# Optimization experiments

Measured on AMD Instinct MI355X. Metric: run time of the kernel, lower is better.

The kernel has to match this reference:

```python
import jax, jax.numpy as jnp
import numpy as np

HIDDEN_SIZE = 2048
NUM_Q_HEADS = 16
NUM_KV_HEADS = 4
HEAD_DIM = 128
EPS = 1e-6
B, T = 1, 4096


def rms_norm(x, w):
    xf = x.astype(jnp.float32)
    n = xf * jax.lax.rsqrt(jnp.mean(xf * xf, axis=-1, keepdims=True) + EPS)
    return (n * w.astype(jnp.float32)).astype(x.dtype)


def rotate_half(x):
    x1, x2 = jnp.split(x, 2, axis=-1)
    return jnp.concatenate([-x2, x1], axis=-1)


def apply_rope(x, cos, sin):
    # x: [B, H, T, D]; cos/sin: [B, T, D]
    return x * cos[:, None, :, :] + rotate_half(x) * sin[:, None, :, :]


def setup_inputs() -> dict:
    key = jax.random.key(0)
    ks = jax.random.split(key, 6)
    s = 0.02
    x = jax.random.normal(ks[0], (B, T, HIDDEN_SIZE), dtype=jnp.float32)
    position_ids = jnp.arange(T, dtype=jnp.int64 if jax.config.jax_enable_x64 else jnp.int32)[None, :].repeat(B, axis=0)
    inv_freq = (1.0 / (10000.0 ** (np.arange(0, HEAD_DIM, 2, dtype=np.float32) / HEAD_DIM))).astype(np.float32)
    inv_freq = jnp.asarray(inv_freq)
    Wq = jax.random.normal(ks[1], (HIDDEN_SIZE, NUM_Q_HEADS * HEAD_DIM * 2), dtype=jnp.float32) * s
    Wk = jax.random.normal(ks[2], (HIDDEN_SIZE, NUM_KV_HEADS * HEAD_DIM), dtype=jnp.float32) * s
    Wv = jax.random.normal(ks[3], (HIDDEN_SIZE, NUM_KV_HEADS * HEAD_DIM), dtype=jnp.float32) * s
    Wo = jax.random.normal(ks[4], (NUM_Q_HEADS * HEAD_DIM, HIDDEN_SIZE), dtype=jnp.float32) * s
    q_norm_w = jnp.ones((HEAD_DIM,), dtype=jnp.float32)
    k_norm_w = jnp.ones((HEAD_DIM,), dtype=jnp.float32)
    return {"x": x, "position_ids": position_ids, "inv_freq": inv_freq,
            "Wq": Wq, "Wk": Wk, "Wv": Wv, "Wo": Wo,
            "q_norm_w": q_norm_w, "k_norm_w": k_norm_w}


def reference(x, position_ids, inv_freq, Wq, Wk, Wv, Wo, q_norm_w, k_norm_w):
    Bb, Tt, _ = x.shape
    dtype = x.dtype
    qg = (x @ Wq).reshape(Bb, Tt, NUM_Q_HEADS, HEAD_DIM * 2)
    q, gate = qg[..., :HEAD_DIM], qg[..., HEAD_DIM:]
    gate = gate.reshape(Bb, Tt, NUM_Q_HEADS * HEAD_DIM)
    k = (x @ Wk).reshape(Bb, Tt, NUM_KV_HEADS, HEAD_DIM)
    v = (x @ Wv).reshape(Bb, Tt, NUM_KV_HEADS, HEAD_DIM)
    q = rms_norm(q, q_norm_w)
    k = rms_norm(k, k_norm_w)
    q = q.transpose(0, 2, 1, 3)  # [B, Hq, T, D]
    k = k.transpose(0, 2, 1, 3)  # [B, Hkv, T, D]
    v = v.transpose(0, 2, 1, 3)
    # RoPE angles: [B, T, D/2] -> concat -> [B, T, D]
    freqs = position_ids.astype(jnp.float32)[:, :, None] * inv_freq[None, None, :]
    emb = jnp.concatenate([freqs, freqs], axis=-1)
    cos, sin = jnp.cos(emb).astype(dtype), jnp.sin(emb).astype(dtype)
    q = apply_rope(q, cos, sin)
    k = apply_rope(k, cos, sin)
    groups = NUM_Q_HEADS // NUM_KV_HEADS
    k = jnp.repeat(k, groups, axis=1)  # [B, Hq, T, D]
    v = jnp.repeat(v, groups, axis=1)
    scale = HEAD_DIM ** -0.5
    attn = jnp.einsum('bhqd,bhkd->bhqk', q, k) * scale
    causal = jnp.tril(jnp.ones((Tt, Tt), dtype=bool))
    attn = jnp.where(causal[None, None, :, :], attn, jnp.array(-jnp.inf, dtype=attn.dtype))
    attn = jax.nn.softmax(attn.astype(jnp.float32), axis=-1).astype(dtype)
    out = jnp.einsum('bhqk,bhkd->bhqd', attn, v)
    out = out.transpose(0, 2, 1, 3).reshape(Bb, Tt, NUM_Q_HEADS * HEAD_DIM)
    out = out * jax.nn.sigmoid(gate)
    return out @ Wo
```

## Files before the change

### kernel.cpp

```cpp
#include <hip/hip_runtime.h>
#include <hip/hip_bf16.h>

#define T_SEQ 4096
#define HID 2048
#define NQH 16
#define NKVH 4
#define HD 128
#define KVW (NKVH * HD)
#define KVSTRIDE 1024
#define QGW (NQH * HD * 2)

typedef __attribute__((ext_vector_type(8))) short short8;
typedef __attribute__((ext_vector_type(4))) float f32x4;
typedef __attribute__((ext_vector_type(16))) float f32x16;
typedef __hip_bfloat16 bf16;

__device__ inline float bf2f(bf16 v) { return __bfloat162float(v); }
__device__ inline bf16 f2bf(float v) { return __float2bfloat16(v); }

__device__ inline void storeC(float* p, float v) { *p = v; }
__device__ inline void storeC(bf16* p, float v) { *p = f2bf(v); }

#if __has_builtin(__builtin_amdgcn_exp2f)
__device__ inline float fexp2(float x) { return __builtin_amdgcn_exp2f(x); }
#else
extern "C" __device__ float __ocml_native_exp2_f32(float);
__device__ inline float fexp2(float x) { return __ocml_native_exp2_f32(x); }
#endif

__device__ inline void gload16(const void* g, void* l) {
    __builtin_amdgcn_global_load_lds(
        (const __attribute__((address_space(1))) void*)g,
        (__attribute__((address_space(3))) void*)l, 16, 0, 0);
}

__device__ inline unsigned pack2(float a, float b) {
    union { bf16 h[2]; unsigned u; } x;
    x.h[0] = f2bf(a); x.h[1] = f2bf(b);
    return x.u;
}
union U8 { unsigned u[4]; short8 s; };

__global__ void prep_all(const float* __restrict__ x, bf16* __restrict__ bx,
                         const int* __restrict__ pos, const float* __restrict__ inv_freq,
                         float* __restrict__ cosT, float* __restrict__ sinT,
                         const float* __restrict__ Wq, const float* __restrict__ Wk,
                         const float* __restrict__ Wv, const float* __restrict__ Wo,
                         bf16* __restrict__ bWq, bf16* __restrict__ bKV,
                         bf16* __restrict__ bWo) {
    __shared__ float tile[32][33];
    const int b = blockIdx.x, tid = threadIdx.x;
    if (b < 8192) {
        int id = (b * 256 + tid) * 4;
        float4 v = *(const float4*)(x + id);
        bf16 tmp[4] = {f2bf(v.x), f2bf(v.y), f2bf(v.z), f2bf(v.w)};
        *(uint2*)(bx + id) = *(uint2*)tmp;
        return;
    }
    if (b < 9216) {
        int id = (b - 8192) * 256 + tid;
        int t = id >> 6, i = id & 63;
        float f = (float)pos[t] * inv_freq[i];
        cosT[id] = cosf(f);
        sinT[id] = sinf(f);
        return;
    }
    const int tx = tid & 31, ty = tid >> 5;
    const float* src; bf16* dst; int C, cs, r0;
    if (b < 19456) {
        int idx = b - 9216;
        int c0 = (idx % 160) * 32;
        r0 = (idx / 160) * 32;
        if (c0 < QGW)            { src = Wq; dst = bWq; C = QGW; cs = c0; }
        else if (c0 < QGW + KVW) { src = Wk; dst = bKV; C = KVW; cs = c0 - QGW; }
        else                     { src = Wv; dst = bKV + (long)KVW * HID; C = KVW; cs = c0 - QGW - KVW; }
    } else {
        int idx = b - 19456;
        cs = (idx % 64) * 32;
        r0 = (idx / 64) * 32;
        src = Wo; dst = bWo; C = HID;
    }
#pragma unroll
    for (int k = 0; k < 4; ++k)
        tile[ty + 8 * k][tx] = src[(long)(r0 + ty + 8 * k) * C + cs + tx];
    __syncthreads();
#pragma unroll
    for (int k = 0; k < 4; ++k)
        dst[(long)(cs + ty + 8 * k) * HID + r0 + tx] = f2bf(tile[tx][ty + 8 * k]);
}

__global__ void mid_prep(bf16* __restrict__ qg, bf16* __restrict__ kvb, bf16* __restrict__ vT,
                         const float* __restrict__ qw, const float* __restrict__ kw,
                         const float* __restrict__ cosT, const float* __restrict__ sinT,
                         float qScale) {
    __shared__ bf16 tile[32][33];
    const int b = blockIdx.x, tid = threadIdx.x;
    if (b < 2048) {
        const int tx = tid & 31, ty = tid >> 5;
        const int d0 = (b & 15) * 32, t0 = (b >> 4) * 32;
#pragma unroll
        for (int k = 0; k < 4; ++k)
            tile[ty + 8 * k][tx] = kvb[(long)(t0 + ty + 8 * k) * KVSTRIDE + KVW + d0 + tx];
        __syncthreads();
#pragma unroll
        for (int k = 0; k < 4; ++k)
            vT[(long)(d0 + ty + 8 * k) * T_SEQ + t0 + tx] = tile[tx][ty + 8 * k];
        return;
    }
    const int bb = b - 2048;
    const int sub = tid >> 6, lane = tid & 63;
    const int NQB = (T_SEQ * NQH) / 4;
    bf16* p; const float* w; float sc; int t;
    if (bb < NQB) {
        int row = bb * 4 + sub;
        t = row >> 4;
        int h = row & 15;
        p = qg + (long)t * QGW + h * (HD * 2);
        w = qw; sc = qScale;
    } else {
        int row = (bb - NQB) * 4 + sub;
        t = row >> 2;
        int h = row & 3;
        p = kvb + (long)t * KVSTRIDE + h * HD;
        w = kw; sc = 1.0f;
    }
    float x1 = bf2f(p[lane]), x2 = bf2f(p[lane + 64]);
    float ss = x1 * x1 + x2 * x2;
    ss += __shfl_xor(ss, 1);
    ss += __shfl_xor(ss, 2);
    ss += __shfl_xor(ss, 4);
    ss += __shfl_xor(ss, 8);
    ss += __shfl_xor(ss, 16);
    ss += __shfl_xor(ss, 32);
    float r = rsqrtf(ss * (1.0f / 128.0f) + 1e-6f);
    float c = cosT[t * 64 + lane], s = sinT[t * 64 + lane];
    float n1 = x1 * r * w[lane], n2 = x2 * r * w[lane + 64];
    p[lane] = f2bf((n1 * c - n2 * s) * sc);
    p[lane + 64] = f2bf((n2 * c + n1 * s) * sc);
}

template <typename OutT>
__global__ __launch_bounds__(256) void gemm_bt(const bf16* __restrict__ A,
                                               const bf16* __restrict__ Bt,
                                               OutT* __restrict__ C, int M, int N, int K) {
    __shared__ __align__(16) bf16 As[128 * 32];
    __shared__ __align__(16) bf16 Bs[128 * 32];
    const int tid = threadIdx.x, lane = tid & 63, wv = tid >> 6;
    const int nwg = gridDim.x * gridDim.y;
    const int orig = blockIdx.y * gridDim.x + blockIdx.x;
    const int wg = (orig & 7) * (nwg >> 3) + (orig >> 3);
    const int bm = (wg / gridDim.x) * 128, bn = (wg % gridDim.x) * 128;
    const int wm = (wv >> 1) * 64, wn = (wv & 1) * 64;
    const int lr = lane & 15, lg = lane >> 4;
    f32x4 acc[4][4] = {};
    const int srow = tid >> 2, skg = (tid & 3) * 8;
    const bf16* aP = A + (long)(bm + srow) * K + skg;
    const bf16* bP = Bt + (long)(bn + srow) * K + skg;
    bf16* asBase = As + wv * 512;
    bf16* bsBase = Bs + wv * 512;
    for (int kt = 0; kt < K; kt += 32) {
        __syncthreads();
        gload16(aP + kt, asBase);
        gload16(aP + (long)64 * K + kt, asBase + 2048);
        gload16(bP + kt, bsBase);
        gload16(bP + (long)64 * K + kt, bsBase + 2048);
        __syncthreads();
        short8 af[4], bfv[4];
#pragma unroll
        for (int m = 0; m < 4; ++m)
            af[m] = *(const short8*)(As + (wm + m * 16 + lr) * 32 + lg * 8);
#pragma unroll
        for (int n = 0; n < 4; ++n)
            bfv[n] = *(const short8*)(Bs + (wn + n * 16 + lr) * 32 + lg * 8);
#pragma unroll
        for (int m = 0; m < 4; ++m)
#pragma unroll
            for (int n = 0; n < 4; ++n)
                acc[m][n] = __builtin_amdgcn_mfma_f32_16x16x32_bf16(af[m], bfv[n], acc[m][n], 0, 0, 0);
    }
#pragma unroll
    for (int m = 0; m < 4; ++m)
#pragma unroll
        for (int n = 0; n < 4; ++n)
#pragma unroll
            for (int j = 0; j < 4; ++j) {
                int r = bm + wm + m * 16 + lg * 4 + j;
                int c = bn + wn + n * 16 + lr;
                storeC(&C[(long)r * N + c], acc[m][n][j]);
            }
}

template <int BN, typename OutT>
__global__ __launch_bounds__(512, 2) void gemm256(const bf16* __restrict__ A,
                                                  const bf16* __restrict__ Bt,
                                                  OutT* __restrict__ C, int M, int N, int K) {
    constexpr int FN = BN / 64;
    __shared__ __align__(16) bf16 As[2][256 * 64];
    __shared__ __align__(16) bf16 Bs[2][BN * 64];
    const int tid = threadIdx.x, lane = tid & 63, wv = tid >> 6;
    const int wr = wv >> 2, wc = wv & 3;
    const int lr = lane & 15, lg = lane >> 4;
    const int nwg = gridDim.x * gridDim.y;
    const int flat = blockIdx.y * gridDim.x + blockIdx.x;
    const int wg = (flat & 7) * (nwg >> 3) + (flat >> 3);
    const int bm = (wg / gridDim.x) * 256, bn = (wg % gridDim.x) * BN;
    const int nt = K >> 6;

    const int srow = tid >> 3, sslot = tid & 7;
    const int slotLog = sslot ^ (srow & 7);
    const bf16* aSrc = A + (long)(bm + srow) * K + slotLog * 8;
    const bf16* bSrc = Bt + (long)(bn + srow) * K + slotLog * 8;

    auto stageA = [&](int T, int hh) {
        const int b_ = T & 1;
        gload16(aSrc + (long)(hh * 128) * K + (long)T * 64, &As[b_][hh * 8192 + wv * 512]);
        gload16(aSrc + (long)(hh * 128 + 64) * K + (long)T * 64, &As[b_][hh * 8192 + 4096 + wv * 512]);
    };
    auto stageB = [&](int T, int hh) {
        const int b_ = T & 1;
        gload16(bSrc + (long)(hh * 128) * K + (long)T * 64, &Bs[b_][hh * 8192 + wv * 512]);
        gload16(bSrc + (long)(hh * 128 + 64) * K + (long)T * 64, &Bs[b_][hh * 8192 + 4096 + wv * 512]);
    };

    int slotE[2];
#pragma unroll
    for (int ks = 0; ks < 2; ++ks) slotE[ks] = ((ks * 4 + lg) ^ (lr & 7)) * 8;

    f32x4 acc[8][FN] = {};

    stageB(0, 0);
    if constexpr (BN == 256) stageB(0, 1);
    stageA(0, 0); stageA(0, 1);
    stageB(1, 0);
    if constexpr (BN == 256) stageB(1, 1);
    if constexpr (BN == 256) asm volatile("s_waitcnt vmcnt(4)" ::: "memory");
    else                     asm volatile("s_waitcnt vmcnt(2)" ::: "memory");
    __builtin_amdgcn_s_barrier();

    for (int t = 0; t < nt; ++t) {
        const int cur = t & 1;
        const bf16* Acur = As[cur];
        const bf16* Bcur = Bs[cur];
        short8 bfr[FN * 2];
#pragma unroll
        for (int q = 0; q < 4; ++q) {
            if (q == 0) {
#pragma unroll
                for (int fn = 0; fn < FN; ++fn)
#pragma unroll
                    for (int ks = 0; ks < 2; ++ks)
                        bfr[fn * 2 + ks] =
                            *(const short8*)(Bcur + (wc * (BN / 4) + fn * 16 + lr) * 64 + slotE[ks]);
            }
            short8 afr[4];
#pragma unroll
            for (int f2 = 0; f2 < 2; ++f2)
#pragma unroll
                for (int ks = 0; ks < 2; ++ks)
                    afr[f2 * 2 + ks] =
                        *(const short8*)(Acur + (wr * 128 + (q * 2 + f2) * 16 + lr) * 64 + slotE[ks]);
            if (q == 0) { if (t + 1 < nt) stageA(t + 1, 0); }
            else if (q == 1) { if (t + 1 < nt) stageA(t + 1, 1); }
            else if (q == 2) { if (t + 2 < nt) stageB(t + 2, 0); }
            else { if (BN == 256 && t + 2 < nt) stageB(t + 2, 1); }
            __builtin_amdgcn_s_barrier();
            __builtin_amdgcn_s_setprio(1);
#pragma unroll
            for (int f2 = 0; f2 < 2; ++f2)
#pragma unroll
                for (int fn = 0; fn < FN; ++fn)
#pragma unroll
                    for (int ks = 0; ks < 2; ++ks)
                        acc[q * 2 + f2][fn] = __builtin_amdgcn_mfma_f32_16x16x32_bf16(
                            afr[f2 * 2 + ks], bfr[fn * 2 + ks], acc[q * 2 + f2][fn], 0, 0, 0);
            __builtin_amdgcn_s_setprio(0);
            if (q == 3) {
                if constexpr (BN == 256) asm volatile("s_waitcnt vmcnt(4)" ::: "memory");
                else                     asm volatile("s_waitcnt vmcnt(2)" ::: "memory");
            }
            __builtin_amdgcn_s_barrier();
        }
    }

#pragma unroll
    for (int fm = 0; fm < 8; ++fm)
#pragma unroll
        for (int fn = 0; fn < FN; ++fn)
#pragma unroll
            for (int j = 0; j < 4; ++j) {
                int r = bm + wr * 128 + fm * 16 + lg * 4 + j;
                int c = bn + wc * (BN / 4) + fn * 16 + lr;
                storeC(&C[(long)r * N + c], acc[fm][fn][j]);
            }
}

__global__ __launch_bounds__(256, 2) void attn9(const bf16* __restrict__ qg,
                                                const bf16* __restrict__ kvb,
                                                const bf16* __restrict__ vT,
                                                bf16* __restrict__ aout) {
    __shared__ __align__(16) bf16 Ks[2][64 * 128];
    __shared__ __align__(16) bf16 Vs[2][128 * 64];
    const int tid = threadIdx.x, lane = tid & 63, wv = tid >> 6;
    const int q32 = lane & 31, g = lane >> 5;
    const int bid = blockIdx.x;
    const int xcd = bid & 7, slot = bid >> 3;
    const int h = 2 * xcd + (slot & 1);
    const int chunk = 31 - (slot >> 1);
    const int hk = h >> 2;
    const int q0w = chunk * 128 + wv * 32;
    const int nkt = 2 * chunk + 2;
    const int qr = q0w + q32;

    short8 bq[8];
    {
        const bf16* qp = qg + (long)(q0w + q32) * QGW + h * (HD * 2) + g * 8;
#pragma unroll
        for (int kk = 0; kk < 8; ++kk) bq[kk] = *(const short8*)(qp + kk * 16);
    }

    f32x16 acc[4] = {};
    f32x16 accL = {};
    float m2 = -1e30f;
    const short8 vONE = {16256, 16256, 16256, 16256, 16256, 16256, 16256, 16256};

    const bf16* kS[4];
    const bf16* vS[4];
    int kOff[4], vOff[4];
#pragma unroll
    for (int i = 0; i < 4; ++i) {
        const int kc = wv * 4 + i;
        const int krow = kc * 4 + (lane >> 4);
        const int kcolB = ((lane & 15) * 16) ^ ((krow & 15) << 4);
        kS[i] = kvb + (long)krow * KVSTRIDE + hk * HD + (kcolB >> 1);
        kOff[i] = kc * 512;
        const int vc = wv * 4 + i;
        const int vrow = vc * 8 + (lane >> 3);
        const int vcolB = ((lane & 7) * 16) ^ ((vrow & 7) << 4);
        vS[i] = vT + (long)(hk * HD + vrow) * T_SEQ + (vcolB >> 1);
        vOff[i] = vc * 512;
    }

#pragma unroll
    for (int i = 0; i < 4; ++i) gload16(kS[i], &Ks[0][kOff[i]]);
#pragma unroll
    for (int i = 0; i < 4; ++i) gload16(vS[i], &Vs[0][vOff[i]]);
    __syncthreads();

    const int kSlotB = (g * 16) ^ ((q32 & 15) << 4);
    const int vSlotB = (g * 16) ^ ((q32 & 7) << 4);

    for (int kt = 0; kt < nkt; ++kt) {
        const int cur = kt & 1;
        if (kt + 1 < nkt) {
            const long koff = (long)(kt + 1) * 64;
#pragma unroll
            for (int i = 0; i < 4; ++i) gload16(kS[i] + koff * KVSTRIDE, &Ks[cur ^ 1][kOff[i]]);
#pragma unroll
            for (int i = 0; i < 4; ++i) gload16(vS[i] + koff, &Vs[cur ^ 1][vOff[i]]);
        }
        const int key00 = kt * 64;
        if (key00 <= q0w + 31) {
            const bf16* KsB = Ks[cur];
            const bf16* VsB = Vs[cur];
            f32x16 s0 = {}, s1 = {};
#pragma unroll
            for (int kk = 0; kk < 8; ++kk) {
                const int ko = q32 * 128 + (((kk * 32) ^ kSlotB) >> 1);
                short8 ka0 = *(const short8*)(KsB + ko);
                short8 ka1 = *(const short8*)(KsB + ko + 4096);
                s0 = __builtin_amdgcn_mfma_f32_32x32x16_bf16(ka0, bq[kk], s0, 0, 0, 0);
                s1 = __builtin_amdgcn_mfma_f32_32x32x16_bf16(ka1, bq[kk], s1, 0, 0, 0);
            }
            if (key00 + 63 > q0w) {
#pragma unroll
                for (int r = 0; r < 16; ++r) {
                    const int krow = (r & 3) + 8 * (r >> 2) + 4 * g;
                    if (key00 + krow > qr) s0[r] = -1e30f;
                    if (key00 + 32 + krow > qr) s1[r] = -1e30f;
                }
            }
            float t8[8];
#pragma unroll
            for (int i = 0; i < 8; ++i)
                t8[i] = fmaxf(fmaxf(s0[i], s0[i + 8]), fmaxf(s1[i], s1[i + 8]));
            float mx = fmaxf(fmaxf(fmaxf(t8[0], t8[1]), fmaxf(t8[2], t8[3])),
                             fmaxf(fmaxf(t8[4], t8[5]), fmaxf(t8[6], t8[7])));
            mx = fmaxf(mx, __shfl_xor(mx, 32));
            float mn = m2, e = 1.f;
            bool need = false;
            if (mx > m2 + 8.f) { mn = mx; e = fexp2(m2 - mx); need = true; }
            m2 = mn;
#pragma unroll
            for (int r = 0; r < 16; ++r) {
                s0[r] = fexp2(s0[r] - mn);
                s1[r] = fexp2(s1[r] - mn);
            }
            if (__any(need)) {
#pragma unroll
                for (int r = 0; r < 16; ++r) {
                    const int krow = (r & 3) + 8 * (r >> 2) + 4 * g;
                    float er = __shfl(e, krow);
#pragma unroll
                    for (int n = 0; n < 4; ++n) acc[n][r] *= er;
                    accL[r] *= er;
                }
            }
            short8 pa[4];
#pragma unroll
            for (int half = 0; half < 2; ++half) {
                const f32x16& p = half ? s1 : s0;
                unsigned lo0 = pack2(p[0], p[1]),   lo1 = pack2(p[2], p[3]);
                unsigned hi0 = pack2(p[4], p[5]),   hi1 = pack2(p[6], p[7]);
                unsigned lo2 = pack2(p[8], p[9]),   lo3 = pack2(p[10], p[11]);
                unsigned hi2 = pack2(p[12], p[13]), hi3 = pack2(p[14], p[15]);
                unsigned sw0 = __shfl_xor(g ? lo0 : hi0, 32);
                unsigned sw1 = __shfl_xor(g ? lo1 : hi1, 32);
                unsigned sw2 = __shfl_xor(g ? lo2 : hi2, 32);
                unsigned sw3 = __shfl_xor(g ? lo3 : hi3, 32);
                U8 a0, a1;
                a0.u[0] = g ? sw0 : lo0;  a0.u[1] = g ? sw1 : lo1;
                a0.u[2] = g ? hi0 : sw0;  a0.u[3] = g ? hi1 : sw1;
                a1.u[0] = g ? sw2 : lo2;  a1.u[1] = g ? sw3 : lo3;
                a1.u[2] = g ? hi2 : sw2;  a1.u[3] = g ? hi3 : sw3;
                pa[half * 2] = a0.s;
                pa[half * 2 + 1] = a1.s;
            }
#pragma unroll
            for (int ks = 0; ks < 4; ++ks) {
                const int vo = q32 * 64 + (((ks * 32) ^ vSlotB) >> 1);
#pragma unroll
                for (int n = 0; n < 4; ++n) {
                    short8 vb = *(const short8*)(VsB + vo + n * 2048);
                    acc[n] = __builtin_amdgcn_mfma_f32_32x32x16_bf16(pa[ks], vb, acc[n], 0, 0, 0);
                }
                accL = __builtin_amdgcn_mfma_f32_32x32x16_bf16(pa[ks], vONE, accL, 0, 0, 0);
            }
        }
        __syncthreads();
    }

#pragma unroll
    for (int r = 0; r < 16; ++r) {
        const int krow = (r & 3) + 8 * (r >> 2) + 4 * g;
        const float linv = 1.0f / accL[r];
        const long t = q0w + krow;
        const bf16* gp = qg + t * QGW + h * (HD * 2) + HD + q32;
        bf16* op = aout + t * (NQH * HD) + h * HD + q32;
#pragma unroll
        for (int n = 0; n < 4; ++n) {
            float gv = bf2f(gp[n * 32]);
            float o = acc[n][r] * linv * (1.f / (1.f + __expf(-gv)));
            op[n * 32] = f2bf(o);
        }
    }
}

extern "C" void kernel_launch(void* const* d_in, const int* in_sizes, int n_in,
                              void* d_out, int out_size, void* d_ws, size_t ws_size,
                              hipStream_t stream) {
    const float* x = (const float*)d_in[0];
    const int* pos = (const int*)d_in[1];
    const float* inv_freq = (const float*)d_in[2];
    const float* Wq = (const float*)d_in[3];
    const float* Wk = (const float*)d_in[4];
    const float* Wv = (const float*)d_in[5];
    const float* Wo = (const float*)d_in[6];
    const float* qw = (const float*)d_in[7];
    const float* kw = (const float*)d_in[8];
    float* out = (float*)d_out;

    char* ws = (char*)d_ws;
    float* cosT = (float*)ws;               ws += (long)T_SEQ * 64 * 4;
    float* sinT = (float*)ws;               ws += (long)T_SEQ * 64 * 4;
    bf16* bx = (bf16*)ws;                   ws += (long)T_SEQ * HID * 2;
    bf16* bWq = (bf16*)ws;                  ws += (long)QGW * HID * 2;
    bf16* bKV = (bf16*)ws;                  ws += (long)KVSTRIDE * HID * 2;
    bf16* bWo = (bf16*)ws;                  ws += (long)HID * HID * 2;
    bf16* qg = (bf16*)ws;                   ws += (long)T_SEQ * QGW * 2;
    bf16* kvb = (bf16*)ws;                  ws += (long)T_SEQ * KVSTRIDE * 2;
    bf16* aout = (bf16*)ws;                 ws += (long)T_SEQ * (NQH * HD) * 2;
    bf16* vT = (bf16*)bWq;

    prep_all<<<23552, 256, 0, stream>>>(x, bx, pos, inv_freq, cosT, sinT,
                                        Wq, Wk, Wv, Wo, bWq, bKV, bWo);

    gemm256<256, bf16><<<dim3(QGW / 256, T_SEQ / 256), 512, 0, stream>>>(bx, bWq, qg, T_SEQ, QGW, HID);
    gemm_bt<bf16><<<dim3(KVSTRIDE / 128, T_SEQ / 128), 256, 0, stream>>>(bx, bKV, kvb, T_SEQ, KVSTRIDE, HID);

    mid_prep<<<2048 + 20480, 256, 0, stream>>>(qg, kvb, vT, qw, kw, cosT, sinT,
                                               0.08838834764831845f * 1.4426950408889634f);

    attn9<<<dim3(512), 256, 0, stream>>>(qg, kvb, vT, aout);

    gemm256<128, float><<<dim3(HID / 128, T_SEQ / 256), 512, 0, stream>>>(aout, bWo, out, T_SEQ, HID, NQH * HD);
}
```

Measured before the change: 326.7 us.

## Software-pipeline attention QK^T one tile ahead with triple-buffered V

```diff
diff --git a/kernel.cpp b/kernel.cpp
--- a/kernel.cpp
+++ b/kernel.cpp
@@ -294,12 +294,12 @@
             }
 }
 
-__global__ __launch_bounds__(256, 2) void attn9(const bf16* __restrict__ qg,
-                                                const bf16* __restrict__ kvb,
-                                                const bf16* __restrict__ vT,
-                                                bf16* __restrict__ aout) {
+__global__ __launch_bounds__(256, 2) void attn12(const bf16* __restrict__ qg,
+                                                 const bf16* __restrict__ kvb,
+                                                 const bf16* __restrict__ vT,
+                                                 bf16* __restrict__ aout) {
     __shared__ __align__(16) bf16 Ks[2][64 * 128];
-    __shared__ __align__(16) bf16 Vs[2][128 * 64];
+    __shared__ __align__(16) bf16 Vs[3][128 * 64];
     const int tid = threadIdx.x, lane = tid & 63, wv = tid >> 6;
     const int q32 = lane & 31, g = lane >> 5;
     const int bid = blockIdx.x;
@@ -340,49 +340,57 @@
         vOff[i] = vc * 512;
     }
 
-#pragma unroll
-    for (int i = 0; i < 4; ++i) gload16(kS[i], &Ks[0][kOff[i]]);
-#pragma unroll
-    for (int i = 0; i < 4; ++i) gload16(vS[i], &Vs[0][vOff[i]]);
-    __syncthreads();
+    auto stageK = [&](int T, int buf) {
+        const long koff = (long)T * 64;
+#pragma unroll
+        for (int i = 0; i < 4; ++i) gload16(kS[i] + koff * KVSTRIDE, &Ks[buf][kOff[i]]);
+    };
+    auto stageV = [&](int T, int buf) {
+        const long koff = (long)T * 64;
+#pragma unroll
+        for (int i = 0; i < 4; ++i) gload16(vS[i] + koff, &Vs[buf][vOff[i]]);
+    };
 
     const int kSlotB = (g * 16) ^ ((q32 & 15) << 4);
     const int vSlotB = (g * 16) ^ ((q32 & 7) << 4);
 
+    auto computeQK = [&](const bf16* KsB, f32x16& s0, f32x16& s1) {
+#pragma unroll
+        for (int kk = 0; kk < 8; ++kk) {
+            const int ko = q32 * 128 + (((kk * 32) ^ kSlotB) >> 1);
+            short8 ka0 = *(const short8*)(KsB + ko);
+            short8 ka1 = *(const short8*)(KsB + ko + 4096);
+            s0 = __builtin_amdgcn_mfma_f32_32x32x16_bf16(ka0, bq[kk], s0, 0, 0, 0);
+            s1 = __builtin_amdgcn_mfma_f32_32x32x16_bf16(ka1, bq[kk], s1, 0, 0, 0);
+        }
+    };
+
+    stageK(0, 0); stageV(0, 0);
+    __syncthreads();
+    f32x16 s0c = {}, s1c = {};
+    computeQK(Ks[0], s0c, s1c);
+    if (nkt > 1) { stageK(1, 1); stageV(1, 1); }
+
     for (int kt = 0; kt < nkt; ++kt) {
-        const int cur = kt & 1;
-        if (kt + 1 < nkt) {
-            const long koff = (long)(kt + 1) * 64;
-#pragma unroll
-            for (int i = 0; i < 4; ++i) gload16(kS[i] + koff * KVSTRIDE, &Ks[cur ^ 1][kOff[i]]);
-#pragma unroll
-            for (int i = 0; i < 4; ++i) gload16(vS[i] + koff, &Vs[cur ^ 1][vOff[i]]);
-        }
+        __syncthreads();
+        f32x16 s0n = {}, s1n = {};
+        if ((kt + 1 < nkt) && ((kt + 1) * 64 <= q0w + 31))
+            computeQK(Ks[(kt + 1) & 1], s0n, s1n);
+        if (kt + 2 < nkt) { stageK(kt + 2, kt & 1); stageV(kt + 2, (kt + 2) % 3); }
         const int key00 = kt * 64;
         if (key00 <= q0w + 31) {
-            const bf16* KsB = Ks[cur];
-            const bf16* VsB = Vs[cur];
-            f32x16 s0 = {}, s1 = {};
-#pragma unroll
-            for (int kk = 0; kk < 8; ++kk) {
-                const int ko = q32 * 128 + (((kk * 32) ^ kSlotB) >> 1);
-                short8 ka0 = *(const short8*)(KsB + ko);
-                short8 ka1 = *(const short8*)(KsB + ko + 4096);
-                s0 = __builtin_amdgcn_mfma_f32_32x32x16_bf16(ka0, bq[kk], s0, 0, 0, 0);
-                s1 = __builtin_amdgcn_mfma_f32_32x32x16_bf16(ka1, bq[kk], s1, 0, 0, 0);
-            }
             if (key00 + 63 > q0w) {
 #pragma unroll
                 for (int r = 0; r < 16; ++r) {
                     const int krow = (r & 3) + 8 * (r >> 2) + 4 * g;
-                    if (key00 + krow > qr) s0[r] = -1e30f;
-                    if (key00 + 32 + krow > qr) s1[r] = -1e30f;
+                    if (key00 + krow > qr) s0c[r] = -1e30f;
+                    if (key00 + 32 + krow > qr) s1c[r] = -1e30f;
                 }
             }
             float t8[8];
 #pragma unroll
             for (int i = 0; i < 8; ++i)
-                t8[i] = fmaxf(fmaxf(s0[i], s0[i + 8]), fmaxf(s1[i], s1[i + 8]));
+                t8[i] = fmaxf(fmaxf(s0c[i], s0c[i + 8]), fmaxf(s1c[i], s1c[i + 8]));
             float mx = fmaxf(fmaxf(fmaxf(t8[0], t8[1]), fmaxf(t8[2], t8[3])),
                              fmaxf(fmaxf(t8[4], t8[5]), fmaxf(t8[6], t8[7])));
             mx = fmaxf(mx, __shfl_xor(mx, 32));
@@ -392,8 +400,8 @@
             m2 = mn;
 #pragma unroll
             for (int r = 0; r < 16; ++r) {
-                s0[r] = fexp2(s0[r] - mn);
-                s1[r] = fexp2(s1[r] - mn);
+                s0c[r] = fexp2(s0c[r] - mn);
+                s1c[r] = fexp2(s1c[r] - mn);
             }
             if (__any(need)) {
 #pragma unroll
@@ -408,7 +416,7 @@
             short8 pa[4];
 #pragma unroll
             for (int half = 0; half < 2; ++half) {
-                const f32x16& p = half ? s1 : s0;
+                const f32x16& p = half ? s1c : s0c;
                 unsigned lo0 = pack2(p[0], p[1]),   lo1 = pack2(p[2], p[3]);
                 unsigned hi0 = pack2(p[4], p[5]),   hi1 = pack2(p[6], p[7]);
                 unsigned lo2 = pack2(p[8], p[9]),   lo3 = pack2(p[10], p[11]);
@@ -425,6 +433,7 @@
                 pa[half * 2] = a0.s;
                 pa[half * 2 + 1] = a1.s;
             }
+            const bf16* VsB = Vs[kt % 3];
 #pragma unroll
             for (int ks = 0; ks < 4; ++ks) {
                 const int vo = q32 * 64 + (((ks * 32) ^ vSlotB) >> 1);
@@ -436,7 +445,8 @@
                 accL = __builtin_amdgcn_mfma_f32_32x32x16_bf16(pa[ks], vONE, accL, 0, 0, 0);
             }
         }
-        __syncthreads();
+        s0c = s0n;
+        s1c = s1n;
     }
 
 #pragma unroll
@@ -490,7 +500,7 @@
     mid_prep<<<2048 + 20480, 256, 0, stream>>>(qg, kvb, vT, qw, kw, cosT, sinT,
                                                0.08838834764831845f * 1.4426950408889634f);
 
-    attn9<<<dim3(512), 256, 0, stream>>>(qg, kvb, vT, aout);
+    attn12<<<dim3(512), 256, 0, stream>>>(qg, kvb, vT, aout);
 
     gemm256<128, float><<<dim3(HID / 128, T_SEQ / 256), 512, 0, stream>>>(aout, bWo, out, T_SEQ, HID, NQH * HD);
 }
```

Result: faster. 320.0 us (-2.1%).
